# Optimization experiments

Hardware: AMD Instinct MI355X
Metric: run time of the kernel (lower is better)

The kernel has to match this reference:

```python
import jax, jax.numpy as jnp
import numpy as np

B, T, U = 4, 250, 120
EPROJS, DUNITS, EMBED, JOINT, ODIM, ATT = 512, 512, 512, 512, 1024, 512
BLANK = 0


def _p(key, shape, scale=0.02):
    return jax.random.normal(key, shape, dtype=jnp.float32) * scale


def setup_inputs() -> dict:
    key = jax.random.key(0)
    ks = jax.random.split(key, 24)
    hs_pad = jax.random.normal(ks[0], (B, T, EPROJS), dtype=jnp.float32)
    ys_in_pad = jax.random.randint(ks[1], (B, U), 0, ODIM)
    hlens = jax.random.randint(ks[2], (B,), T // 2, T + 1).astype(jnp.int32)
    embed = _p(ks[3], (ODIM, EMBED)).at[BLANK].set(0.0)  # padding_idx=blank
    # LSTMCell layer 0: input = embed + eprojs
    W_ih0 = _p(ks[4], (4 * DUNITS, EMBED + EPROJS)); b_ih0 = jnp.zeros((4 * DUNITS,), jnp.float32)
    W_hh0 = _p(ks[5], (4 * DUNITS, DUNITS));          b_hh0 = jnp.zeros((4 * DUNITS,), jnp.float32)
    # LSTMCell layer 1
    W_ih1 = _p(ks[6], (4 * DUNITS, DUNITS)); b_ih1 = jnp.zeros((4 * DUNITS,), jnp.float32)
    W_hh1 = _p(ks[7], (4 * DUNITS, DUNITS)); b_hh1 = jnp.zeros((4 * DUNITS,), jnp.float32)
    # additive attention (AttAdd): mlp_enc (bias), mlp_dec (no bias), gvec
    W_att_enc = _p(ks[8], (EPROJS, ATT)); b_att_enc = jnp.zeros((ATT,), jnp.float32)
    W_att_dec = _p(ks[9], (DUNITS, ATT))
    gvec = _p(ks[10], (ATT,))
    # joint network
    W_lin_enc = _p(ks[11], (JOINT, EPROJS)); b_lin_enc = jnp.zeros((JOINT,), jnp.float32)
    W_lin_dec = _p(ks[12], (JOINT, DUNITS))  # bias=False
    W_lin_out = _p(ks[13], (ODIM, JOINT));   b_lin_out = jnp.zeros((ODIM,), jnp.float32)
    return dict(hs_pad=hs_pad, ys_in_pad=ys_in_pad, hlens=hlens, embed=embed,
                W_ih0=W_ih0, b_ih0=b_ih0, W_hh0=W_hh0, b_hh0=b_hh0,
                W_ih1=W_ih1, b_ih1=b_ih1, W_hh1=W_hh1, b_hh1=b_hh1,
                W_att_enc=W_att_enc, b_att_enc=b_att_enc, W_att_dec=W_att_dec, gvec=gvec,
                W_lin_enc=W_lin_enc, b_lin_enc=b_lin_enc, W_lin_dec=W_lin_dec,
                W_lin_out=W_lin_out, b_lin_out=b_lin_out)


def _lstm_cell(x, h, c, W_ih, b_ih, W_hh, b_hh):
    g = x @ W_ih.T + b_ih + h @ W_hh.T + b_hh
    i, f, gg, o = jnp.split(g, 4, axis=-1)  # torch gate order: i, f, g, o
    c_new = jax.nn.sigmoid(f) * c + jax.nn.sigmoid(i) * jnp.tanh(gg)
    h_new = jax.nn.sigmoid(o) * jnp.tanh(c_new)
    return h_new, c_new


def reference(hs_pad, ys_in_pad, hlens, embed,
              W_ih0, b_ih0, W_hh0, b_hh0, W_ih1, b_ih1, W_hh1, b_hh1,
              W_att_enc, b_att_enc, W_att_dec, gvec,
              W_lin_enc, b_lin_enc, W_lin_dec, W_lin_out, b_lin_out):
    Bq, Tq = hs_pad.shape[0], hs_pad.shape[1]
    eys = embed[ys_in_pad]  # (B, U, E)
    pre_enc = hs_pad @ W_att_enc + b_att_enc  # (B, T, A), computed once
    mask = jnp.arange(Tq)[None, :] < hlens[:, None]  # (B, T)

    def step(carry, ey_i):
        z0, c0, z1, c1 = carry
        # additive attention: scores over encoder frames
        q = z0 @ W_att_dec  # (B, A)
        e = jnp.tanh(pre_enc + q[:, None, :]) @ gvec  # (B, T)
        e = jnp.where(mask, e, -1e9)
        w = jax.nn.softmax(e, axis=-1)
        att_c = jnp.einsum('bt,btd->bd', w, hs_pad)  # (B, eprojs)
        ey = jnp.concatenate([ey_i, att_c], axis=1)  # (B, E+eprojs)
        z0n, c0n = _lstm_cell(ey, z0, c0, W_ih0, b_ih0, W_hh0, b_hh0)
        z1n, c1n = _lstm_cell(z0n, z1, c1, W_ih1, b_ih1, W_hh1, b_hh1)
        return (z0n, c0n, z1n, c1n), z1n

    zeros = jnp.zeros((Bq, DUNITS), hs_pad.dtype)
    _, ys = jax.lax.scan(step, (zeros, zeros, zeros, zeros),
                         jnp.swapaxes(eys, 0, 1))  # ys: (U, B, D)
    h_dec = jnp.swapaxes(ys, 0, 1)  # (B, U, D)

    # joint: broadcast add of enc/dec projections, tanh, output proj
    henc = hs_pad @ W_lin_enc.T + b_lin_enc  # (B, T, J)
    hdec = h_dec @ W_lin_dec.T               # (B, U, J)
    z = jnp.tanh(henc[:, :, None, :] + hdec[:, None, :, :])  # (B, T, U, J)
    return z @ W_lin_out.T + b_lin_out  # (B, T, U, odim)
```

## Files before the change

kernel.cpp:

```cpp
#include <hip/hip_runtime.h>

#define B_ 4
#define T_ 250
#define U_ 120
#define D_ 512
#define G_ 2048
#define O_ 1024
#define NBLK 256

typedef __attribute__((ext_vector_type(8))) short bf16x8;
typedef __attribute__((ext_vector_type(4))) float f32x4;
typedef __attribute__((ext_vector_type(4))) unsigned int ui4;

__device__ __forceinline__ float tanh_fast(float x){
  float e = __expf(2.f*x);
  return 1.f - 2.f/(e + 1.f);
}
__device__ __forceinline__ float sigmoid_fast(float x){
  return 1.f/(1.f + __expf(-x));
}
__device__ __forceinline__ unsigned short f2bf(float x){
  unsigned int u = __float_as_uint(x);
  unsigned int r = (u + 0x7FFFu + ((u >> 16) & 1u)) >> 16;
  return (unsigned short)r;
}

__device__ __forceinline__ void atomStoreF(float* p, float v){
  __hip_atomic_store(p, v, __ATOMIC_RELAXED, __HIP_MEMORY_SCOPE_AGENT);
}
__device__ __forceinline__ void mall_load4f(const float* p0, const float* p1,
    const float* p2, const float* p3, float& v0, float& v1, float& v2, float& v3){
  asm volatile(
    "global_load_dword %0, %4, off sc0 sc1\n\t"
    "global_load_dword %1, %5, off sc0 sc1\n\t"
    "global_load_dword %2, %6, off sc0 sc1\n\t"
    "global_load_dword %3, %7, off sc0 sc1\n\t"
    "s_waitcnt vmcnt(0)"
    : "=&v"(v0), "=&v"(v1), "=&v"(v2), "=&v"(v3)
    : "v"(p0), "v"(p1), "v"(p2), "v"(p3)
    : "memory");
}

__device__ __forceinline__ void gbar_arrive(int* flags, int gen){
  __syncthreads();
  if (threadIdx.x == 0){
    asm volatile("s_waitcnt vmcnt(0)" ::: "memory");
    __hip_atomic_store(&flags[blockIdx.x*16], gen, __ATOMIC_RELAXED,
                       __HIP_MEMORY_SCOPE_AGENT);
  }
}
__device__ __forceinline__ void gbar_wait(int* flags, int* rel, int gen){
  if (blockIdx.x == 0){
    if (threadIdx.x < 64){
      int l = threadIdx.x;
      const int* p0 = flags + (l*4+0)*16;
      const int* p1 = flags + (l*4+1)*16;
      const int* p2 = flags + (l*4+2)*16;
      const int* p3 = flags + (l*4+3)*16;
      long c = 0;
      while (true){
        int f0,f1,f2,f3;
        asm volatile(
          "global_load_dword %0, %4, off sc0 sc1\n\t"
          "global_load_dword %1, %5, off sc0 sc1\n\t"
          "global_load_dword %2, %6, off sc0 sc1\n\t"
          "global_load_dword %3, %7, off sc0 sc1\n\t"
          "s_waitcnt vmcnt(0)"
          : "=&v"(f0),"=&v"(f1),"=&v"(f2),"=&v"(f3)
          : "v"(p0), "v"(p1), "v"(p2), "v"(p3)
          : "memory");
        int m0 = f0 < f1 ? f0 : f1;
        int m1 = f2 < f3 ? f2 : f3;
        int mm = m0 < m1 ? m0 : m1;
        if (__all(mm >= gen)) break;
        if (++c > (1L<<22)) break;
      }
      if (threadIdx.x == 0)
        __hip_atomic_store(rel, gen, __ATOMIC_RELAXED,
                           __HIP_MEMORY_SCOPE_AGENT);
    }
  } else {
    if (threadIdx.x == 0){
      long c = 0;
      while (__hip_atomic_load(rel, __ATOMIC_RELAXED,
                               __HIP_MEMORY_SCOPE_AGENT) < gen){
        if (++c > (1L<<22)) break;
      }
    }
  }
  __syncthreads();
}
__device__ __forceinline__ void gbar(int* flags, int* rel, int gen){
  gbar_arrive(flags, gen);
  gbar_wait(flags, rel, gen);
}

__global__ void gather_embed_k(const int* __restrict__ ys, const float* __restrict__ embed,
                               float* __restrict__ eys, int* __restrict__ flags){
  int i = blockIdx.x*256 + threadIdx.x;
  if (i < NBLK*16 + 16)
    __hip_atomic_store(&flags[i], 0, __ATOMIC_RELAXED, __HIP_MEMORY_SCOPE_AGENT);
  if (i < B_*U_*D_){
    int r = i >> 9, k = i & 511;
    eys[i] = embed[ys[r]*D_ + k];
  }
}

__device__ __forceinline__ void gemm64_nt_body(float* smem,
  const float* __restrict__ A, int lda, const float* __restrict__ B, int ldb,
  const float* __restrict__ bias, float* __restrict__ C, int ldc,
  int M, int N, int K, int bx, int by)
{
  float (*As)[65] = (float(*)[65])smem;
  float (*Bs)[65] = (float(*)[65])(smem + 16*65);
  int tid = threadIdx.x;
  int m0 = by*64, n0 = bx*64;
  int tx = tid & 15, ty = tid >> 4;
  float acc[4][4] = {};
  for (int k0 = 0; k0 < K; k0 += 16){
#pragma unroll
    for (int i=0;i<4;i++){
      int e = tid + 256*i;
      int mm = e >> 4, kk = e & 15;
      int mg = m0 + mm;
      As[kk][mm] = (mg < M) ? A[(size_t)mg*lda + k0 + kk] : 0.f;
      int ng = n0 + mm;
      Bs[kk][mm] = (ng < N) ? B[(size_t)ng*ldb + k0 + kk] : 0.f;
    }
    __syncthreads();
#pragma unroll
    for (int kk=0;kk<16;kk++){
      float av[4], bv[4];
#pragma unroll
      for (int i=0;i<4;i++) av[i] = As[kk][ty*4+i];
#pragma unroll
      for (int j=0;j<4;j++) bv[j] = Bs[kk][tx*4+j];
#pragma unroll
      for (int i=0;i<4;i++)
#pragma unroll
        for (int j=0;j<4;j++) acc[i][j] += av[i]*bv[j];
    }
    __syncthreads();
  }
#pragma unroll
  for (int i=0;i<4;i++){
    int m = m0 + ty*4 + i;
    if (m < M){
#pragma unroll
      for (int j=0;j<4;j++){
        int n = n0 + tx*4 + j;
        if (n < N) C[(size_t)m*ldc + n] = acc[i][j] + (bias ? bias[n] : 0.f);
      }
    }
  }
}

__device__ __forceinline__ void gemm64_nn_body(float* smem,
  const float* __restrict__ A, int lda, const float* __restrict__ B, int ldb,
  const float* __restrict__ bias, float* __restrict__ C, int ldc,
  int M, int N, int K, int bx, int by)
{
  float (*As)[65] = (float(*)[65])smem;
  float (*Bs)[65] = (float(*)[65])(smem + 16*65);
  int tid = threadIdx.x;
  int m0 = by*64, n0 = bx*64;
  int tx = tid & 15, ty = tid >> 4;
  float acc[4][4] = {};
  for (int k0 = 0; k0 < K; k0 += 16){
#pragma unroll
    for (int i=0;i<4;i++){
      int e = tid + 256*i;
      int mm = e >> 4, kk = e & 15;
      int mg = m0 + mm;
      As[kk][mm] = (mg < M) ? A[(size_t)mg*lda + k0 + kk] : 0.f;
      int nn = e & 63, kk2 = e >> 6;
      int ng = n0 + nn;
      Bs[kk2][nn] = (ng < N) ? B[(size_t)(k0+kk2)*ldb + ng] : 0.f;
    }
    __syncthreads();
#pragma unroll
    for (int kk=0;kk<16;kk++){
      float av[4], bv[4];
#pragma unroll
      for (int i=0;i<4;i++) av[i] = As[kk][ty*4+i];
#pragma unroll
      for (int j=0;j<4;j++) bv[j] = Bs[kk][tx*4+j];
#pragma unroll
      for (int i=0;i<4;i++)
#pragma unroll
        for (int j=0;j<4;j++) acc[i][j] += av[i]*bv[j];
    }
    __syncthreads();
  }
#pragma unroll
  for (int i=0;i<4;i++){
    int m = m0 + ty*4 + i;
    if (m < M){
#pragma unroll
      for (int j=0;j<4;j++){
        int n = n0 + tx*4 + j;
        if (n < N) C[(size_t)m*ldc + n] = acc[i][j] + (bias ? bias[n] : 0.f);
      }
    }
  }
}

__global__ __launch_bounds__(256) void pre_gemms_k(
  const float* __restrict__ hs, const float* __restrict__ eys,
  const float* __restrict__ W_att_enc, const float* __restrict__ b_att_enc,
  const float* __restrict__ W_lin_enc, const float* __restrict__ b_lin_enc,
  const float* __restrict__ W_ih0,
  float* __restrict__ pre_enc, float* __restrict__ henc,
  float* __restrict__ pre0, float* __restrict__ hsW0)
{
  __shared__ float smem[2*16*65];
  int id = blockIdx.x;
  if (id < 128){
    gemm64_nn_body(smem, hs,512, W_att_enc,512, b_att_enc, pre_enc,512,
                   B_*T_,512,512, id & 7, id >> 3);
  } else if (id < 256){
    id -= 128;
    gemm64_nt_body(smem, hs,512, W_lin_enc,512, b_lin_enc, henc,512,
                   B_*T_,512,512, id & 7, id >> 3);
  } else if (id < 512){
    id -= 256;
    gemm64_nt_body(smem, eys,512, W_ih0,1024, nullptr, pre0,2048,
                   B_*U_,2048,512, id & 31, id >> 5);
  } else {
    id -= 512;
    gemm64_nt_body(smem, hs,512, W_ih0+512,1024, nullptr, hsW0,2048,
                   B_*T_,2048,512, id & 31, id >> 5);
  }
}

__global__ __launch_bounds__(256) void gemm64_nt_k(
  const float* __restrict__ A, int lda, const float* __restrict__ B, int ldb,
  const float* __restrict__ bias, float* __restrict__ C, int ldc,
  int M, int N, int K)
{
  __shared__ float smem[2*16*65];
  gemm64_nt_body(smem, A,lda,B,ldb,bias,C,ldc,M,N,K, blockIdx.x, blockIdx.y);
}

__global__ __launch_bounds__(256) void scan_k(
    float* __restrict__ z0, float* __restrict__ z1,
    float* __restrict__ q,  float* __restrict__ e,
    int* __restrict__ flags, int* __restrict__ rel,
    const float* __restrict__ pre_enc, const float* __restrict__ pre0,
    const float* __restrict__ hsW0,
    const float* __restrict__ W_hh0, const float* __restrict__ W_ih1,
    const float* __restrict__ W_hh1, const float* __restrict__ W_att_dec,
    const float* __restrict__ gvec, const int* __restrict__ hlens,
    const float* __restrict__ b_ih0, const float* __restrict__ b_hh0,
    const float* __restrict__ b_ih1, const float* __restrict__ b_hh1,
    float* __restrict__ h_dec)
{
  int bk = blockIdx.x, tid = threadIdx.x;
  int lane = tid & 63, wv = tid >> 6;
  int d0 = bk * 2;

  __shared__ float whh0_s[8*512];
  __shared__ float whh1_s[8*512];
  __shared__ float wih1_s[8*512];
  __shared__ float wdec_s[2*512];
  __shared__ float hsw_s[4*8*256];
  __shared__ float pre0_s[480*8];
  __shared__ float pre_s[4*512];
  __shared__ float gvec_s[512];
  __shared__ float zs0[2048], zs1[2048], qs[2048];
  __shared__ float pA0[32], pA1[32], gB[32], gC[32];
  __shared__ float bias0_s[8], bias1_s[8], c0_s[8], c1_s[8];
  __shared__ int hlens_s[4];

  for (int idx = tid; idx < 8*512; idx += 256){
    int gd = idx >> 9, k = idx & 511;
    int j = (gd >> 1)*512 + d0 + (gd & 1);
    whh0_s[idx] = W_hh0[(size_t)j*512 + k];
    whh1_s[idx] = W_hh1[(size_t)j*512 + k];
    wih1_s[idx] = W_ih1[(size_t)j*512 + k];
  }
  for (int idx = tid; idx < 2*512; idx += 256){
    int dd = idx >> 9, k = idx & 511;
    wdec_s[idx] = W_att_dec[(size_t)k*512 + d0 + dd];
  }
  for (int idx = tid; idx < 4*1000; idx += 256){
    int gp = idx & 3, tg = idx >> 2;
    int b = tg / 250, t = tg - b*250;
    const float2 v = *(const float2*)(hsW0 + (size_t)tg*G_ + gp*512 + d0);
    hsw_s[(b*8 + gp*2 + 0)*256 + t] = v.x;
    hsw_s[(b*8 + gp*2 + 1)*256 + t] = v.y;
  }
  for (int idx = tid; idx < 4*8*6; idx += 256){
    int t = 250 + (idx % 6), bg = idx / 6;
    hsw_s[bg*256 + t] = 0.f;
  }
  for (int idx = tid; idx < 480*4; idx += 256){
    int gp = idx & 3, r = idx >> 2;
    const float2 v = *(const float2*)(pre0 + (size_t)r*G_ + gp*512 + d0);
    pre0_s[r*8 + gp*2 + 0] = v.x;
    pre0_s[r*8 + gp*2 + 1] = v.y;
  }
  for (int idx = tid; idx < 4*512; idx += 256){
    int r = bk*4 + (idx >> 9);
    pre_s[idx] = (r < B_*T_) ? pre_enc[(size_t)r*512 + (idx & 511)] : 0.f;
  }
  for (int idx = tid; idx < 512; idx += 256) gvec_s[idx] = gvec[idx];
  for (int idx = tid; idx < 2048; idx += 256) zs0[idx] = 0.f;
  if (tid < 4) hlens_s[tid] = hlens[tid];
  if (tid < 32){ pA0[tid] = 0.f; }
  if (tid < 8){
    int j = ((tid >> 1))*512 + d0 + (tid & 1);
    bias0_s[tid] = b_ih0[j] + b_hh0[j];
    bias1_s[tid] = b_ih1[j] + b_hh1[j];
    c0_s[tid] = 0.f; c1_s[tid] = 0.f;
    int b = tid >> 1, d = d0 + (tid & 1);
    atomStoreF(&z1[b*512 + d], 0.f);
    atomStoreF(&q [b*512 + d], 0.f);
  }
  int gen = 0;
  gbar(flags, rel, ++gen);

  for (int u = 0; u < U_; ++u){
    {
      float vz[8], vq[8];
#pragma unroll
      for (int i=0;i<8;i++)
        asm volatile("global_load_dword %0, %1, off sc0 sc1"
                     : "=&v"(vz[i]) : "v"(&z1[tid + 256*i]));
#pragma unroll
      for (int i=0;i<8;i++)
        asm volatile("global_load_dword %0, %1, off sc0 sc1"
                     : "=&v"(vq[i]) : "v"(&q[tid + 256*i]));
      asm volatile("s_waitcnt vmcnt(0)" ::: "memory");
#pragma unroll
      for (int i=0;i<8;i++){ zs1[tid + 256*i] = vz[i]; qs[tid + 256*i] = vq[i]; }
    }
    __syncthreads();
    {
      int r = bk*4 + wv;
      if (r < B_*T_){
        int b = r / 250, t = r - b*250;
        float s = 0.f;
#pragma unroll
        for (int i=0;i<8;i++){
          int k = i*64 + lane;
          float x = pre_s[wv*512+k] + qs[b*512+k];
          s += tanh_fast(x) * gvec_s[k];
        }
#pragma unroll
        for (int off=32; off; off>>=1) s += __shfl_xor(s, off);
        if (lane == 0) atomStoreF(&e[r], (t < hlens_s[b]) ? s : -1e30f);
      }
    }
    gbar_arrive(flags, ++gen);
    {
      int gd0 = wv*2, gd1 = wv*2 + 1;
      float a10[4]={}, a11[4]={};
#pragma unroll
      for (int i = 0; i < 8; ++i){
        int k = i*64 + lane;
        float w10 = whh1_s[gd0*512+k], w11 = whh1_s[gd1*512+k];
#pragma unroll
        for (int b=0;b<4;b++){
          float zv1 = zs1[b*512+k];
          a10[b] += w10*zv1; a11[b] += w11*zv1;
        }
      }
#pragma unroll
      for (int b=0;b<4;b++){
#pragma unroll
        for (int off=32; off; off>>=1){
          a10[b] += __shfl_xor(a10[b],off); a11[b] += __shfl_xor(a11[b],off);
        }
      }
      if (lane == 0){
#pragma unroll
        for (int b=0;b<4;b++){ pA1[b*8+gd0] = a10[b]; pA1[b*8+gd1] = a11[b]; }
      }
    }
    gbar_wait(flags, rel, gen);
    {
      int b = wv;
      const float* eb = e + b*250;
      float vals[4], w_reg[4];
      int t3 = 192 + lane;
      mall_load4f(eb + lane, eb + 64 + lane, eb + 128 + lane,
                  eb + (t3 < 250 ? t3 : 249),
                  vals[0], vals[1], vals[2], vals[3]);
      if (t3 >= 250) vals[3] = -1e30f;
      float vmax = fmaxf(fmaxf(vals[0],vals[1]), fmaxf(vals[2],vals[3]));
#pragma unroll
      for (int off=32; off; off>>=1) vmax = fmaxf(vmax, __shfl_xor(vmax, off));
      float ssum = 0.f;
#pragma unroll
      for (int i=0;i<4;i++){
        int t = i*64 + lane;
        w_reg[i] = (t < 250) ? __expf(vals[i] - vmax) : 0.f;
        ssum += w_reg[i];
      }
#pragma unroll
      for (int off=32; off; off>>=1) ssum += __shfl_xor(ssum, off);
      float inv = 1.f / ssum;
#pragma unroll
      for (int i=0;i<4;i++) w_reg[i] *= inv;

      float ag[8] = {};
#pragma unroll
      for (int i=0;i<4;i++){
        int t = i*64 + lane;
#pragma unroll
        for (int gd=0; gd<8; gd++)
          ag[gd] += w_reg[i] * hsw_s[(b*8+gd)*256 + t];
      }
#pragma unroll
      for (int gd=0; gd<8; gd++){
#pragma unroll
        for (int off=32; off; off>>=1) ag[gd] += __shfl_xor(ag[gd], off);
      }
      if (lane == 0){
#pragma unroll
        for (int gd=0; gd<8; gd++)
          gB[b*8+gd] = ag[gd] + pA0[b*8+gd] + pre0_s[(b*U_+u)*8 + gd] + bias0_s[gd];
      }
    }
    __syncthreads();
    if (tid < 8){
      int b = tid >> 1, dd = tid & 1;
      float ig = sigmoid_fast(gB[b*8 + 0 + dd]);
      float fg = sigmoid_fast(gB[b*8 + 2 + dd]);
      float gg = tanh_fast  (gB[b*8 + 4 + dd]);
      float og = sigmoid_fast(gB[b*8 + 6 + dd]);
      float cn = fg * c0_s[tid] + ig * gg;
      c0_s[tid] = cn;
      atomStoreF(&z0[b*512 + d0 + dd], og * tanh_fast(cn));
    }
    gbar(flags, rel, ++gen);
    {
      float vza[8];
#pragma unroll
      for (int i=0;i<8;i++)
        asm volatile("global_load_dword %0, %1, off sc0 sc1"
                     : "=&v"(vza[i]) : "v"(&z0[tid + 256*i]));
      asm volatile("s_waitcnt vmcnt(0)" ::: "memory");
#pragma unroll
      for (int i=0;i<8;i++) zs0[tid + 256*i] = vza[i];
    }
    __syncthreads();
    {
      int gd0 = wv*2, gd1 = wv*2 + 1;
      float a0[4]={}, a1[4]={};
#pragma unroll
      for (int i=0;i<8;i++){
        int k = i*64 + lane;
        float w0 = wih1_s[gd0*512+k], w1 = wih1_s[gd1*512+k];
#pragma unroll
        for (int b=0;b<4;b++){
          float zv = zs0[b*512+k];
          a0[b] += w0*zv; a1[b] += w1*zv;
        }
      }
#pragma unroll
      for (int b=0;b<4;b++){
#pragma unroll
        for (int off=32; off; off>>=1){
          a0[b] += __shfl_xor(a0[b],off); a1[b] += __shfl_xor(a1[b],off);
        }
      }
      if (lane == 0){
#pragma unroll
        for (int b=0;b<4;b++){
          gC[b*8+gd0] = a0[b] + pA1[b*8+gd0] + bias1_s[gd0];
          gC[b*8+gd1] = a1[b] + pA1[b*8+gd1] + bias1_s[gd1];
        }
      }
      if (wv < 2){
        float qa[4] = {};
#pragma unroll
        for (int i=0;i<8;i++){
          int k = i*64 + lane;
          float wq = wdec_s[wv*512+k];
#pragma unroll
          for (int b=0;b<4;b++) qa[b] += wq * zs0[b*512+k];
        }
#pragma unroll
        for (int b=0;b<4;b++){
#pragma unroll
          for (int off=32; off; off>>=1) qa[b] += __shfl_xor(qa[b],off);
        }
        if (lane == 0){
#pragma unroll
          for (int b=0;b<4;b++) atomStoreF(&q[b*512 + d0 + wv], qa[b]);
        }
      }
    }
    __syncthreads();
    if (tid < 8){
      int b = tid >> 1, dd = tid & 1;
      float ig = sigmoid_fast(gC[b*8 + 0 + dd]);
      float fg = sigmoid_fast(gC[b*8 + 2 + dd]);
      float gg = tanh_fast  (gC[b*8 + 4 + dd]);
      float og = sigmoid_fast(gC[b*8 + 6 + dd]);
      float cn = fg * c1_s[tid] + ig * gg;
      c1_s[tid] = cn;
      float hn = og * tanh_fast(cn);
      atomStoreF(&z1[b*512 + d0 + dd], hn);
      h_dec[((size_t)(b*U_ + u))*512 + d0 + dd] = hn;
    }
    gbar_arrive(flags, ++gen);
    {
      int gd0 = wv*2, gd1 = wv*2 + 1;
      float a00[4]={}, a01[4]={};
#pragma unroll
      for (int i = 0; i < 8; ++i){
        int k = i*64 + lane;
        float w00 = whh0_s[gd0*512+k], w01 = whh0_s[gd1*512+k];
#pragma unroll
        for (int b=0;b<4;b++){
          float zv0 = zs0[b*512+k];
          a00[b] += w00*zv0; a01[b] += w01*zv0;
        }
      }
#pragma unroll
      for (int b=0;b<4;b++){
#pragma unroll
        for (int off=32; off; off>>=1){
          a00[b] += __shfl_xor(a00[b],off); a01[b] += __shfl_xor(a01[b],off);
        }
      }
      if (lane == 0){
#pragma unroll
        for (int b=0;b<4;b++){ pA0[b*8+gd0] = a00[b]; pA0[b*8+gd1] = a01[b]; }
      }
    }
    gbar_wait(flags, rel, gen);
  }
}

__global__ __launch_bounds__(256) void pack_k(
    const float* __restrict__ henc, const float* __restrict__ hdec,
    unsigned short* __restrict__ P,
    const float* __restrict__ Wlin, unsigned short* __restrict__ Wb)
{
  const int NP8 = B_*T_*U_*512/8;
  int i = blockIdx.x*256 + threadIdx.x;
  if (i < NP8){
    int e = i*8;
    int k = e & 511;
    int r = e >> 9;
    int u = r % U_;
    int bt = r / U_;
    int b = bt / T_;
    const float* hp = henc + (size_t)bt*512 + k;
    const float* dp = hdec + (size_t)(b*U_ + u)*512 + k;
    unsigned int w[4];
#pragma unroll
    for (int j=0;j<4;j++){
      unsigned short lo = f2bf(tanh_fast(hp[2*j]   + dp[2*j]));
      unsigned short hi = f2bf(tanh_fast(hp[2*j+1] + dp[2*j+1]));
      w[j] = (unsigned int)lo | ((unsigned int)hi << 16);
    }
    *(ui4*)(P + e) = ui4{w[0], w[1], w[2], w[3]};
  } else {
    int j8 = i - NP8;
    if (j8 < O_*512/8){
      int e = j8*8;
      unsigned int w[4];
#pragma unroll
      for (int j=0;j<4;j++){
        unsigned short lo = f2bf(Wlin[e+2*j]);
        unsigned short hi = f2bf(Wlin[e+2*j+1]);
        w[j] = (unsigned int)lo | ((unsigned int)hi << 16);
      }
      *(ui4*)(Wb + e) = ui4{w[0], w[1], w[2], w[3]};
    }
  }
}

__global__ __launch_bounds__(256) void joint_mfma_k(
    const unsigned short* __restrict__ P,
    const unsigned short* __restrict__ Wb,
    const float* __restrict__ bout,
    float* __restrict__ out)
{
  __shared__ __align__(16) char smraw[65536];
  float* outb = (float*)smraw;
  int tid = threadIdx.x;
  int lane = tid & 63;
  int w = tid >> 6, wr = w >> 1, wc = w & 1;
  int id = blockIdx.x;
  int bt = id % 1000;
  int ot = id / 1000;
  int o0 = ot * 128;
  const char* Pbase = (const char*)(P + (size_t)bt*U_*512);
  const char* Wbase = (const char*)(Wb + (size_t)o0*512);

  f32x4 acc[4][4] = {};

#define JSTAGE(bufofs, k0q) \
  { _Pragma("unroll") \
    for (int j=0;j<4;j++){ \
      int pos = (j*256 + tid)*16; \
      int row = pos >> 7; \
      int inrow = pos & 127; \
      int srcin = inrow ^ ((row & 7) << 4); \
      int arow = row < U_ ? row : (U_-1); \
      __builtin_amdgcn_global_load_lds( \
        (const __attribute__((address_space(1))) void*)(Pbase + (size_t)arow*1024 + (k0q)*2 + srcin), \
        (__attribute__((address_space(3))) void*)(smraw + (bufofs) + pos), 16, 0, 0); \
      __builtin_amdgcn_global_load_lds( \
        (const __attribute__((address_space(1))) void*)(Wbase + (size_t)row*1024 + (k0q)*2 + srcin), \
        (__attribute__((address_space(3))) void*)(smraw + (bufofs) + 16384 + pos), 16, 0, 0); \
    } }

  int cur = 0;
  JSTAGE(0, 0);
  asm volatile("s_waitcnt vmcnt(0)" ::: "memory");
  __syncthreads();
#pragma unroll
  for (int t = 0; t < 8; ++t){
    if (t < 7) JSTAGE(cur ^ 32768, (t+1)*64);
    const char* As = smraw + cur;
    const char* Bs = smraw + cur + 16384;
#pragma unroll
    for (int kk=0; kk<2; kk++){
      bf16x8 a[4], bb[4];
#pragma unroll
      for (int m=0;m<4;m++){
        int row = wr*64 + m*16 + (lane & 15);
        int inrow = (kk*64 + (lane >> 4)*16) ^ ((row & 7) << 4);
        a[m] = *(const bf16x8*)(As + row*128 + inrow);
      }
#pragma unroll
      for (int n=0;n<4;n++){
        int row = wc*64 + n*16 + (lane & 15);
        int inrow = (kk*64 + (lane >> 4)*16) ^ ((row & 7) << 4);
        bb[n] = *(const bf16x8*)(Bs + row*128 + inrow);
      }
#pragma unroll
      for (int m=0;m<4;m++)
#pragma unroll
        for (int n=0;n<4;n++)
          acc[m][n] = __builtin_amdgcn_mfma_f32_16x16x32_bf16(a[m], bb[n], acc[m][n], 0, 0, 0);
    }
    asm volatile("s_waitcnt vmcnt(0)" ::: "memory");
    __syncthreads();
    cur ^= 32768;
  }
#undef JSTAGE

  float bv[4];
#pragma unroll
  for (int n=0;n<4;n++) bv[n] = bout[o0 + wc*64 + n*16 + (lane & 15)];
#pragma unroll
  for (int m=0;m<4;m++){
    __syncthreads();
#pragma unroll
    for (int n=0;n<4;n++){
      int col = wc*64 + n*16 + (lane & 15);
      int r0 = wr*16 + ((lane >> 4) << 2);
#pragma unroll
      for (int r=0;r<4;r++)
        outb[(r0+r)*132 + col] = acc[m][n][r] + bv[n];
    }
    __syncthreads();
    int row = tid >> 3;
    int c0  = (tid & 7) * 16;
    int u = (row < 16) ? (m*16 + row) : (64 + m*16 + (row - 16));
    if (u < U_){
      float* op = out + ((size_t)bt*U_ + u)*O_ + o0 + c0;
      const float* sp = &outb[row*132 + c0];
#pragma unroll
      for (int i=0;i<4;i++) *(f32x4*)(op + 4*i) = *(const f32x4*)(sp + 4*i);
    }
  }
}

extern "C" void kernel_launch(void* const* d_in, const int* in_sizes, int n_in,
                              void* d_out, int out_size, void* d_ws, size_t ws_size,
                              hipStream_t stream) {
  const float* hs       = (const float*)d_in[0];
  const int*   ys       = (const int*)  d_in[1];
  const int*   hlens    = (const int*)  d_in[2];
  const float* embed    = (const float*)d_in[3];
  const float* W_ih0    = (const float*)d_in[4];
  const float* b_ih0    = (const float*)d_in[5];
  const float* W_hh0    = (const float*)d_in[6];
  const float* b_hh0    = (const float*)d_in[7];
  const float* W_ih1    = (const float*)d_in[8];
  const float* b_ih1    = (const float*)d_in[9];
  const float* W_hh1    = (const float*)d_in[10];
  const float* b_hh1    = (const float*)d_in[11];
  const float* W_att_enc= (const float*)d_in[12];
  const float* b_att_enc= (const float*)d_in[13];
  const float* W_att_dec= (const float*)d_in[14];
  const float* gvec     = (const float*)d_in[15];
  const float* W_lin_enc= (const float*)d_in[16];
  const float* b_lin_enc= (const float*)d_in[17];
  const float* W_lin_dec= (const float*)d_in[18];
  const float* W_lin_out= (const float*)d_in[19];
  const float* b_lin_out= (const float*)d_in[20];
  float* out = (float*)d_out;

  float* w = (float*)d_ws;
  float* z0      = w;
  float* z1      = w + 2048;
  float* q       = w + 4096;
  float* e       = w + 6144;
  int*   flags   = (int*)(w + 7168);
  int*   rel     = flags + NBLK*16;
  float* eys     = w + 11776;
  float* pre_enc = w + 257536;
  float* pre0    = w + 769536;
  float* henc    = w + 1752576;
  float* h_dec   = w + 2264576;
  float* hdec_p  = w + 2510336;
  float* hsW0    = w + 2756096;
  unsigned short* Pbf = (unsigned short*)(w + 4804096);
  unsigned short* Wbf = (unsigned short*)(w + 4804096 + 30720000);

  gather_embed_k<<<(B_*U_*D_ + 255)/256, 256, 0, stream>>>(ys, embed, eys, flags);
  pre_gemms_k<<<1024, 256, 0, stream>>>(hs, eys, W_att_enc, b_att_enc,
                                        W_lin_enc, b_lin_enc, W_ih0,
                                        pre_enc, henc, pre0, hsW0);

  {
    void* args[] = {
      (void*)&z0, (void*)&z1, (void*)&q, (void*)&e, (void*)&flags, (void*)&rel,
      (void*)&pre_enc, (void*)&pre0, (void*)&hsW0,
      (void*)&W_hh0, (void*)&W_ih1, (void*)&W_hh1, (void*)&W_att_dec,
      (void*)&gvec, (void*)&hlens,
      (void*)&b_ih0, (void*)&b_hh0, (void*)&b_ih1, (void*)&b_hh1,
      (void*)&h_dec
    };
    hipLaunchCooperativeKernel((const void*)scan_k, dim3(NBLK), dim3(256),
                               args, 0, stream);
  }

  gemm64_nt_k<<<dim3(8, 8), 256, 0, stream>>>(h_dec, 512, W_lin_dec, 512, nullptr,
                                              hdec_p, 512, B_*U_, 512, 512);
  {
    const int NP8 = B_*T_*U_*512/8;
    const int NW8 = O_*512/8;
    pack_k<<<(NP8 + NW8 + 255)/256, 256, 0, stream>>>(henc, hdec_p, Pbf,
                                                      W_lin_out, Wbf);
  }
  joint_mfma_k<<<8000, 256, 0, stream>>>(Pbf, Wbf, b_lin_out, out);
}
```

Baseline: 1.900 ms.

## Fuse embed gather, W_lin_dec projection and weight packing into existing kernels

Removes the separate embedding-gather kernel by reading embedding rows directly inside the pre0 GEMM, moves the W_lin_out bf16 packing and flag reset into extra blocks of pre_gemms_k, and computes the decoder projection (h_dec @ W_lin_dec^T) inside the cooperative scan, placed in the slack between a barrier's arrive and wait. This drops two kernel launches and the h_dec intermediate round trip. The cost is extra shared memory and per-step work in the latency-critical scan loop, plus a tail computation for the final step.

```diff
diff --git a/kernel.cpp b/kernel.cpp
--- a/kernel.cpp
+++ b/kernel.cpp
@@ -95,17 +95,6 @@
   gbar_wait(flags, rel, gen);
 }
 
-__global__ void gather_embed_k(const int* __restrict__ ys, const float* __restrict__ embed,
-                               float* __restrict__ eys, int* __restrict__ flags){
-  int i = blockIdx.x*256 + threadIdx.x;
-  if (i < NBLK*16 + 16)
-    __hip_atomic_store(&flags[i], 0, __ATOMIC_RELAXED, __HIP_MEMORY_SCOPE_AGENT);
-  if (i < B_*U_*D_){
-    int r = i >> 9, k = i & 511;
-    eys[i] = embed[ys[r]*D_ + k];
-  }
-}
-
 __device__ __forceinline__ void gemm64_nt_body(float* smem,
   const float* __restrict__ A, int lda, const float* __restrict__ B, int ldb,
   const float* __restrict__ bias, float* __restrict__ C, int ldc,
@@ -155,6 +144,62 @@
   }
 }
 
+__device__ __forceinline__ void gemm64_nt_embed_body(float* smem,
+  const int* __restrict__ ys, const float* __restrict__ embed,
+  const float* __restrict__ B, int ldb,
+  float* __restrict__ C, int ldc,
+  int M, int N, int K, int bx, int by)
+{
+  float (*As)[65] = (float(*)[65])smem;
+  float (*Bs)[65] = (float(*)[65])(smem + 16*65);
+  int tid = threadIdx.x;
+  int m0 = by*64, n0 = bx*64;
+  int tx = tid & 15, ty = tid >> 4;
+  int yrow[4];
+#pragma unroll
+  for (int i=0;i<4;i++){
+    int e = tid + 256*i;
+    int mg = m0 + (e >> 4);
+    yrow[i] = (mg < M) ? ys[mg] : -1;
+  }
+  float acc[4][4] = {};
+  for (int k0 = 0; k0 < K; k0 += 16){
+#pragma unroll
+    for (int i=0;i<4;i++){
+      int e = tid + 256*i;
+      int mm = e >> 4, kk = e & 15;
+      As[kk][mm] = (yrow[i] >= 0) ? embed[(size_t)yrow[i]*512 + k0 + kk] : 0.f;
+      int ng = n0 + mm;
+      Bs[kk][mm] = (ng < N) ? B[(size_t)ng*ldb + k0 + kk] : 0.f;
+    }
+    __syncthreads();
+#pragma unroll
+    for (int kk=0;kk<16;kk++){
+      float av[4], bv[4];
+#pragma unroll
+      for (int i=0;i<4;i++) av[i] = As[kk][ty*4+i];
+#pragma unroll
+      for (int j=0;j<4;j++) bv[j] = Bs[kk][tx*4+j];
+#pragma unroll
+      for (int i=0;i<4;i++)
+#pragma unroll
+        for (int j=0;j<4;j++) acc[i][j] += av[i]*bv[j];
+    }
+    __syncthreads();
+  }
+#pragma unroll
+  for (int i=0;i<4;i++){
+    int m = m0 + ty*4 + i;
+    if (m < M){
+#pragma unroll
+      for (int j=0;j<4;j++){
+        int n = n0 + tx*4 + j;
+        if (n < N) C[(size_t)m*ldc + n] = acc[i][j];
+      }
+    }
+  }
+}
+
 __device__ __forceinline__ void gemm64_nn_body(float* smem,
   const float* __restrict__ A, int lda, const float* __restrict__ B, int ldb,
   const float* __restrict__ bias, float* __restrict__ C, int ldc,
@@ -206,10 +251,13 @@
 }
 
 __global__ __launch_bounds__(256) void pre_gemms_k(
-  const float* __restrict__ hs, const float* __restrict__ eys,
+  const float* __restrict__ hs, const int* __restrict__ ys,
+  const float* __restrict__ embed,
   const float* __restrict__ W_att_enc, const float* __restrict__ b_att_enc,
   const float* __restrict__ W_lin_enc, const float* __restrict__ b_lin_enc,
   const float* __restrict__ W_ih0,
+  const float* __restrict__ W_lin_out, unsigned short* __restrict__ Wbf,
+  int* __restrict__ flags,
   float* __restrict__ pre_enc, float* __restrict__ henc,
   float* __restrict__ pre0, float* __restrict__ hsW0)
 {
@@ -224,22 +272,32 @@
                    B_*T_,512,512, id & 7, id >> 3);
   } else if (id < 512){
     id -= 256;
-    gemm64_nt_body(smem, eys,512, W_ih0,1024, nullptr, pre0,2048,
-                   B_*U_,2048,512, id & 31, id >> 5);
-  } else {
+    gemm64_nt_embed_body(smem, ys, embed, W_ih0,1024, pre0,2048,
+                         B_*U_,2048,512, id & 31, id >> 5);
+  } else if (id < 1024){
     id -= 512;
     gemm64_nt_body(smem, hs,512, W_ih0+512,1024, nullptr, hsW0,2048,
                    B_*T_,2048,512, id & 31, id >> 5);
-  }
-}
-
-__global__ __launch_bounds__(256) void gemm64_nt_k(
-  const float* __restrict__ A, int lda, const float* __restrict__ B, int ldb,
-  const float* __restrict__ bias, float* __restrict__ C, int ldc,
-  int M, int N, int K)
-{
-  __shared__ float smem[2*16*65];
-  gemm64_nt_body(smem, A,lda,B,ldb,bias,C,ldc,M,N,K, blockIdx.x, blockIdx.y);
+  } else {
+    int tid = threadIdx.x;
+    if (id == 1024){
+      for (int i = tid; i < NBLK*16 + 16; i += 256)
+        __hip_atomic_store(&flags[i], 0, __ATOMIC_RELAXED,
+                           __HIP_MEMORY_SCOPE_AGENT);
+    }
+    int i = (id - 1024)*256 + tid;
+    for (int j8 = i; j8 < O_*512/8; j8 += 8192){
+      int e = j8*8;
+      unsigned int w[4];
+#pragma unroll
+      for (int j=0;j<4;j++){
+        unsigned short lo = f2bf(W_lin_out[e+2*j]);
+        unsigned short hi = f2bf(W_lin_out[e+2*j+1]);
+        w[j] = (unsigned int)lo | ((unsigned int)hi << 16);
+      }
+      *(ui4*)(Wbf + e) = ui4{w[0], w[1], w[2], w[3]};
+    }
+  }
 }
 
 __global__ __launch_bounds__(256) void scan_k(
@@ -250,10 +308,11 @@
     const float* __restrict__ hsW0,
     const float* __restrict__ W_hh0, const float* __restrict__ W_ih1,
     const float* __restrict__ W_hh1, const float* __restrict__ W_att_dec,
+    const float* __restrict__ W_lin_dec,
     const float* __restrict__ gvec, const int* __restrict__ hlens,
     const float* __restrict__ b_ih0, const float* __restrict__ b_hh0,
     const float* __restrict__ b_ih1, const float* __restrict__ b_hh1,
-    float* __restrict__ h_dec)
+    float* __restrict__ hdec_p)
 {
   int bk = blockIdx.x, tid = threadIdx.x;
   int lane = tid & 63, wv = tid >> 6;
@@ -263,6 +322,7 @@
   __shared__ float whh1_s[8*512];
   __shared__ float wih1_s[8*512];
   __shared__ float wdec_s[2*512];
+  __shared__ float wld_s[2*512];
   __shared__ float hsw_s[4*8*256];
   __shared__ float pre0_s[480*8];
   __shared__ float pre_s[4*512];
@@ -282,6 +342,7 @@
   for (int idx = tid; idx < 2*512; idx += 256){
     int dd = idx >> 9, k = idx & 511;
     wdec_s[idx] = W_att_dec[(size_t)k*512 + d0 + dd];
+    wld_s[idx]  = W_lin_dec[(size_t)(d0+dd)*512 + k];
   }
   for (int idx = tid; idx < 4*1000; idx += 256){
     int gp = idx & 3, tg = idx >> 2;
@@ -434,7 +495,28 @@
       c0_s[tid] = cn;
       atomStoreF(&z0[b*512 + d0 + dd], og * tanh_fast(cn));
     }
-    gbar(flags, rel, ++gen);
+    gbar_arrive(flags, ++gen);
+    if (u > 0){
+      int b = wv;
+      float a0 = 0.f, a1 = 0.f;
+#pragma unroll
+      for (int i=0;i<8;i++){
+        int k = i*64 + lane;
+        float zv = zs1[b*512+k];
+        a0 += zv * wld_s[k];
+        a1 += zv * wld_s[512+k];
+      }
+#pragma unroll
+      for (int off=32; off; off>>=1){
+        a0 += __shfl_xor(a0,off); a1 += __shfl_xor(a1,off);
+      }
+      if (lane == 0){
+        size_t base = ((size_t)(b*U_ + (u-1)))*512 + d0;
+        hdec_p[base]   = a0;
+        hdec_p[base+1] = a1;
+      }
+    }
+    gbar_wait(flags, rel, gen);
     {
       float vza[8];
 #pragma unroll
@@ -502,9 +584,7 @@
       float og = sigmoid_fast(gC[b*8 + 6 + dd]);
       float cn = fg * c1_s[tid] + ig * gg;
       c1_s[tid] = cn;
-      float hn = og * tanh_fast(cn);
-      atomStoreF(&z1[b*512 + d0 + dd], hn);
-      h_dec[((size_t)(b*U_ + u))*512 + d0 + dd] = hn;
+      atomStoreF(&z1[b*512 + d0 + dd], og * tanh_fast(cn));
     }
     gbar_arrive(flags, ++gen);
     {
@@ -534,46 +614,63 @@
     }
     gbar_wait(flags, rel, gen);
   }
+
+  {
+    float vz[8];
+#pragma unroll
+    for (int i=0;i<8;i++)
+      asm volatile("global_load_dword %0, %1, off sc0 sc1"
+                   : "=&v"(vz[i]) : "v"(&z1[tid + 256*i]));
+    asm volatile("s_waitcnt vmcnt(0)" ::: "memory");
+#pragma unroll
+    for (int i=0;i<8;i++) zs1[tid + 256*i] = vz[i];
+  }
+  __syncthreads();
+  {
+    int b = wv;
+    float a0 = 0.f, a1 = 0.f;
+#pragma unroll
+    for (int i=0;i<8;i++){
+      int k = i*64 + lane;
+      float zv = zs1[b*512+k];
+      a0 += zv * wld_s[k];
+      a1 += zv * wld_s[512+k];
+    }
+#pragma unroll
+    for (int off=32; off; off>>=1){
+      a0 += __shfl_xor(a0,off); a1 += __shfl_xor(a1,off);
+    }
+    if (lane == 0){
+      size_t base = ((size_t)(b*U_ + (U_-1)))*512 + d0;
+      hdec_p[base]   = a0;
+      hdec_p[base+1] = a1;
+    }
+  }
 }
 
 __global__ __launch_bounds__(256) void pack_k(
     const float* __restrict__ henc, const float* __restrict__ hdec,
-    unsigned short* __restrict__ P,
-    const float* __restrict__ Wlin, unsigned short* __restrict__ Wb)
+    unsigned short* __restrict__ P)
 {
   const int NP8 = B_*T_*U_*512/8;
   int i = blockIdx.x*256 + threadIdx.x;
-  if (i < NP8){
-    int e = i*8;
-    int k = e & 511;
-    int r = e >> 9;
-    int u = r % U_;
-    int bt = r / U_;
-    int b = bt / T_;
-    const float* hp = henc + (size_t)bt*512 + k;
-    const float* dp = hdec + (size_t)(b*U_ + u)*512 + k;
-    unsigned int w[4];
-#pragma unroll
-    for (int j=0;j<4;j++){
-      unsigned short lo = f2bf(tanh_fast(hp[2*j]   + dp[2*j]));
-      unsigned short hi = f2bf(tanh_fast(hp[2*j+1] + dp[2*j+1]));
-      w[j] = (unsigned int)lo | ((unsigned int)hi << 16);
-    }
-    *(ui4*)(P + e) = ui4{w[0], w[1], w[2], w[3]};
-  } else {
-    int j8 = i - NP8;
-    if (j8 < O_*512/8){
-      int e = j8*8;
-      unsigned int w[4];
-#pragma unroll
-      for (int j=0;j<4;j++){
-        unsigned short lo = f2bf(Wlin[e+2*j]);
-        unsigned short hi = f2bf(Wlin[e+2*j+1]);
-        w[j] = (unsigned int)lo | ((unsigned int)hi << 16);
-      }
-      *(ui4*)(Wb + e) = ui4{w[0], w[1], w[2], w[3]};
-    }
-  }
+  if (i >= NP8) return;
+  int e = i*8;
+  int k = e & 511;
+  int r = e >> 9;
+  int u = r % U_;
+  int bt = r / U_;
+  int b = bt / T_;
+  const float* hp = henc + (size_t)bt*512 + k;
+  const float* dp = hdec + (size_t)(b*U_ + u)*512 + k;
+  unsigned int w[4];
+#pragma unroll
+  for (int j=0;j<4;j++){
+    unsigned short lo = f2bf(tanh_fast(hp[2*j]   + dp[2*j]));
+    unsigned short hi = f2bf(tanh_fast(hp[2*j+1] + dp[2*j+1]));
+    w[j] = (unsigned int)lo | ((unsigned int)hi << 16);
+  }
+  *(ui4*)(P + e) = ui4{w[0], w[1], w[2], w[3]};
 }
 
 __global__ __launch_bounds__(256) void joint_mfma_k(
@@ -708,19 +805,17 @@
   float* e       = w + 6144;
   int*   flags   = (int*)(w + 7168);
   int*   rel     = flags + NBLK*16;
-  float* eys     = w + 11776;
   float* pre_enc = w + 257536;
   float* pre0    = w + 769536;
   float* henc    = w + 1752576;
-  float* h_dec   = w + 2264576;
   float* hdec_p  = w + 2510336;
   float* hsW0    = w + 2756096;
   unsigned short* Pbf = (unsigned short*)(w + 4804096);
   unsigned short* Wbf = (unsigned short*)(w + 4804096 + 30720000);
 
-  gather_embed_k<<<(B_*U_*D_ + 255)/256, 256, 0, stream>>>(ys, embed, eys, flags);
-  pre_gemms_k<<<1024, 256, 0, stream>>>(hs, eys, W_att_enc, b_att_enc,
+  pre_gemms_k<<<1056, 256, 0, stream>>>(hs, ys, embed, W_att_enc, b_att_enc,
                                         W_lin_enc, b_lin_enc, W_ih0,
+                                        W_lin_out, Wbf, flags,
                                         pre_enc, henc, pre0, hsW0);
 
   {
@@ -728,21 +823,14 @@
       (void*)&z0, (void*)&z1, (void*)&q, (void*)&e, (void*)&flags, (void*)&rel,
       (void*)&pre_enc, (void*)&pre0, (void*)&hsW0,
       (void*)&W_hh0, (void*)&W_ih1, (void*)&W_hh1, (void*)&W_att_dec,
-      (void*)&gvec, (void*)&hlens,
+      (void*)&W_lin_dec, (void*)&gvec, (void*)&hlens,
       (void*)&b_ih0, (void*)&b_hh0, (void*)&b_ih1, (void*)&b_hh1,
-      (void*)&h_dec
+      (void*)&hdec_p
     };
     hipLaunchCooperativeKernel((const void*)scan_k, dim3(NBLK), dim3(256),
                                args, 0, stream);
   }
 
-  gemm64_nt_k<<<dim3(8, 8), 256, 0, stream>>>(h_dec, 512, W_lin_dec, 512, nullptr,
-                                              hdec_p, 512, B_*U_, 512, 512);
-  {
-    const int NP8 = B_*T_*U_*512/8;
-    const int NW8 = O_*512/8;
-    pack_k<<<(NP8 + NW8 + 255)/256, 256, 0, stream>>>(henc, hdec_p, Pbf,
-                                                      W_lin_out, Wbf);
-  }
+  pack_k<<<(B_*T_*U_*512/8 + 255)/256, 256, 0, stream>>>(henc, hdec_p, Pbf);
   joint_mfma_k<<<8000, 256, 0, stream>>>(Pbf, Wbf, b_lin_out, out);
 }
```

Measured after the change: 1.850 ms. 2.6% less time.
